# Performance work log

Hardware: AMD Instinct MI355X
Metric: run time of the kernel (lower is better)

Reference implementation:

```python
import jax, jax.numpy as jnp
import numpy as np

N = 30000      # nodes
IN = 768       # input feature dim
C = 128        # hidden channels (= conv out_dim, = gate dim)
HEADS = 4      # attention heads (TransformerConv and Semantic)
DH = 128       # per-head dim (concat=False -> out_channels)
R = 3          # num relations
E = 80000      # edges per relation
NEG = 0.01     # LeakyReLU slope


def setup_inputs() -> dict:
    key = jax.random.key(0)
    ks = iter(jax.random.split(key, 64))
    def nx(shape):
        return jax.random.normal(next(ks), shape, dtype=jnp.float32) * 0.02
    inp = {}
    inp["x"] = jax.random.normal(next(ks), (N, IN), dtype=jnp.float32)
    inp["edges"] = jax.random.randint(next(ks), (R, 2, E), 0, N, dtype=jnp.int32)
    inp["lin1_W"] = nx((IN, C)); inp["lin1_b"] = jnp.zeros((C,), jnp.float32)
    for l in ("l1", "l2"):
        inp[f"{l}_Wq"] = nx((R, C, HEADS * DH)); inp[f"{l}_bq"] = jnp.zeros((R, HEADS * DH), jnp.float32)
        inp[f"{l}_Wk"] = nx((R, C, HEADS * DH)); inp[f"{l}_bk"] = jnp.zeros((R, HEADS * DH), jnp.float32)
        inp[f"{l}_Wv"] = nx((R, C, HEADS * DH)); inp[f"{l}_bv"] = jnp.zeros((R, HEADS * DH), jnp.float32)
        inp[f"{l}_Ws"] = nx((R, C, DH));         inp[f"{l}_bs"] = jnp.zeros((R, DH), jnp.float32)
        inp[f"{l}_gW"] = nx((C + DH, C));        inp[f"{l}_gb"] = jnp.zeros((C,), jnp.float32)
        inp[f"{l}_sW1"] = nx((HEADS, C, C));     inp[f"{l}_sb1"] = jnp.zeros((HEADS, C), jnp.float32)
        inp[f"{l}_sw2"] = nx((HEADS, C))
    inp["lin2_W"] = nx((C, C)); inp["lin2_b"] = jnp.zeros((C,), jnp.float32)
    inp["clf_W"] = nx((C, 2)); inp["clf_b"] = jnp.zeros((2,), jnp.float32)
    return inp


def lrelu(x):
    return jnp.where(x >= 0, x, NEG * x)


def transformer_conv(x, src, dst, Wq, bq, Wk, bk, Wv, bv, Ws, bs):
    # PyG TransformerConv, heads=HEADS, concat=False (head mean), root_weight=True, eval (no dropout)
    n = x.shape[0]
    q = (x @ Wq + bq).reshape(n, HEADS, DH)
    k = (x @ Wk + bk).reshape(n, HEADS, DH)
    v = (x @ Wv + bv).reshape(n, HEADS, DH)
    logits = (q[dst] * k[src]).sum(-1) / np.sqrt(DH)      # [E, H]
    m = jax.ops.segment_max(logits, dst, num_segments=n)  # scatter-softmax (stable)
    a = jnp.exp(logits - m[dst])
    s = jax.ops.segment_sum(a, dst, num_segments=n)
    alpha = a / s[dst]
    agg = jax.ops.segment_sum(alpha[:, :, None] * v[src], dst, num_segments=n)  # [N, H, DH]
    return agg.mean(axis=1) + x @ Ws + bs


def semantic(Hm, sW1, sb1, sw2):
    # Hm: [N, R, C]; per-head scoring MLP -> softmax over relations -> weighted sum, averaged over heads
    t = jnp.tanh(jnp.einsum('nrc,hco->hnro', Hm, sW1) + sb1[:, None, None, :])  # [H, N, R, C]
    scores = jnp.einsum('hnro,ho->hnr', t, sw2).mean(axis=1)                    # [H, R]
    beta = jax.nn.softmax(scores, axis=-1)
    return jnp.einsum('hr,nrc->nc', beta, Hm) / HEADS


def rgt_layer(x, edges, Wq, bq, Wk, bk, Wv, bv, Ws, bs, gW, gb, sW1, sb1, sw2):
    Hs = []
    for r in range(R):  # small fixed relation loop
        src, dst = edges[r, 0], edges[r, 1]
        U = transformer_conv(x, src, dst, Wq[r], bq[r], Wk[r], bk[r], Wv[r], bv[r], Ws[r], bs[r])
        Z = jax.nn.sigmoid(jnp.concatenate([U, x], axis=1) @ gW + gb)
        Hs.append(jnp.tanh(U) * Z + x * (1.0 - Z))
    Hm = jnp.stack(Hs, axis=1)  # [N, R, C]
    return semantic(Hm, sW1, sb1, sw2)


def reference(x, edges, lin1_W, lin1_b,
              l1_Wq, l1_bq, l1_Wk, l1_bk, l1_Wv, l1_bv, l1_Ws, l1_bs, l1_gW, l1_gb, l1_sW1, l1_sb1, l1_sw2,
              l2_Wq, l2_bq, l2_Wk, l2_bk, l2_Wv, l2_bv, l2_Ws, l2_bs, l2_gW, l2_gb, l2_sW1, l2_sb1, l2_sw2,
              lin2_W, lin2_b, clf_W, clf_b):
    h = lrelu(x @ lin1_W + lin1_b)
    h = rgt_layer(h, edges, l1_Wq, l1_bq, l1_Wk, l1_bk, l1_Wv, l1_bv, l1_Ws, l1_bs, l1_gW, l1_gb, l1_sW1, l1_sb1, l1_sw2)
    h = rgt_layer(h, edges, l2_Wq, l2_bq, l2_Wk, l2_bk, l2_Wv, l2_bv, l2_Ws, l2_bs, l2_gW, l2_gb, l2_sW1, l2_sb1, l2_sw2)
    h = lrelu(h @ lin2_W + lin2_b)
    return h @ clf_W + clf_b
```

## Files before the change

kernel.cpp:

```cpp
#include <hip/hip_runtime.h>
#include <math.h>

#define Nn 30000
#define RR 3
#define EE 80000
#define MT_M 235

#define SAP 72
#define SAP2 136
#define EP_LD 70
#define KBIG 0x40000000

typedef __attribute__((ext_vector_type(8))) short bf16x8;
typedef __attribute__((ext_vector_type(4))) float f32x4;

__device__ __forceinline__ unsigned short f2bf(float f) {
    union { float f; unsigned u; } v; v.f = f;
    unsigned r = v.u + 0x7fff + ((v.u >> 16) & 1);
    return (unsigned short)(r >> 16);
}
__device__ __forceinline__ float fast_tanh(float x) {
    float e = __expf(2.f * x);
    return 1.f - 2.f / (e + 1.f);
}
__device__ __forceinline__ void unpack8(uint4 u, float* f) {
    union { unsigned u; float f; } a;
    a.u = u.x << 16;          f[0] = a.f;
    a.u = u.x & 0xffff0000u;  f[1] = a.f;
    a.u = u.y << 16;          f[2] = a.f;
    a.u = u.y & 0xffff0000u;  f[3] = a.f;
    a.u = u.z << 16;          f[4] = a.f;
    a.u = u.z & 0xffff0000u;  f[5] = a.f;
    a.u = u.w << 16;          f[6] = a.f;
    a.u = u.w & 0xffff0000u;  f[7] = a.f;
}

__device__ __forceinline__ void mfma_core(
    const short* __restrict__ A, int lda,
    const short* __restrict__ A2, int lda2, int ksplit,
    const short* __restrict__ Bt,
    int M, int K, int m0, int n0,
    short* As, short* Bs, f32x4 (&acc)[4][4])
{
    const int t = threadIdx.x;
    const int srow = t >> 3;
    const int scol = (t & 7) << 3;
    const int lane = t & 63;
    const int wave = t >> 6;
    const int wm = (wave >> 1) << 6;
    const int wn = (wave & 1) << 6;
    const int fr = lane & 15;
    const int quad = lane >> 4;

    for (int k0 = 0; k0 < K; k0 += 64) {
        const short* Abase; int kk0, ldax;
        if (k0 < ksplit) { Abase = A;  kk0 = k0;          ldax = lda;  }
        else             { Abase = A2; kk0 = k0 - ksplit; ldax = lda2; }
        #pragma unroll
        for (int rr = 0; rr < 4; rr++) {
            int r = srow + rr * 32;
            int gr = m0 + r;
            bf16x8 va = {0, 0, 0, 0, 0, 0, 0, 0};
            if (gr < M) va = *(const bf16x8*)(Abase + (size_t)gr * ldax + kk0 + scol);
            *(bf16x8*)(As + r * SAP + scol) = va;
        }
        #pragma unroll
        for (int rr = 0; rr < 4; rr++) {
            int r = srow + rr * 32;
            bf16x8 vb = *(const bf16x8*)(Bt + (size_t)(n0 + r) * K + k0 + scol);
            *(bf16x8*)(Bs + r * SAP + scol) = vb;
        }
        __syncthreads();
        #pragma unroll
        for (int kc = 0; kc < 2; kc++) {
            bf16x8 af[4], bfr[4];
            #pragma unroll
            for (int i = 0; i < 4; i++)
                af[i] = *(const bf16x8*)(As + (wm + i * 16 + fr) * SAP + kc * 32 + quad * 8);
            #pragma unroll
            for (int i = 0; i < 4; i++)
                bfr[i] = *(const bf16x8*)(Bs + (wn + i * 16 + fr) * SAP + kc * 32 + quad * 8);
            #pragma unroll
            for (int mi = 0; mi < 4; mi++)
                #pragma unroll
                for (int ni = 0; ni < 4; ni++)
                    acc[mi][ni] = __builtin_amdgcn_mfma_f32_16x16x32_bf16(
                        af[mi], bfr[ni], acc[mi][ni], 0, 0, 0);
        }
        __syncthreads();
    }
}

__global__ __launch_bounds__(256) void gemm_mfma(
    const short* __restrict__ A, int lda,
    const short* __restrict__ A2, int lda2, int ksplit,
    const short* __restrict__ Bt, const float* __restrict__ bias,
    float* __restrict__ C, int ldc, short* __restrict__ Cbf, int ldcbf,
    int M, int K, int act)
{
    __shared__ short As[128 * SAP];
    __shared__ short Bs[128 * SAP];
    f32x4 acc[4][4];
    #pragma unroll
    for (int i = 0; i < 4; i++)
        #pragma unroll
        for (int j = 0; j < 4; j++) acc[i][j] = (f32x4){0.f, 0.f, 0.f, 0.f};
    int m0 = blockIdx.y * 128, n0 = blockIdx.x * 128;
    mfma_core(A, lda, A2, lda2, ksplit, Bt, M, K, m0, n0, As, Bs, acc);

    const int t = threadIdx.x;
    const int lane = t & 63, wave = t >> 6;
    const int wm = (wave >> 1) << 6, wn = (wave & 1) << 6;
    const int fr = lane & 15, quad = lane >> 4;
    float* ws = (float*)As + wave * 16 * EP_LD;
    const int rrow = lane >> 2;
    const int cseg = (lane & 3) << 4;
    #pragma unroll
    for (int mi = 0; mi < 4; mi++) {
        #pragma unroll
        for (int ni = 0; ni < 4; ni++)
            #pragma unroll
            for (int reg = 0; reg < 4; reg++)
                ws[(quad * 4 + reg) * EP_LD + ni * 16 + fr] = acc[mi][ni][reg];
        int gr = m0 + wm + mi * 16 + rrow;
        if (gr >= M) continue;
        int gc = n0 + wn + cseg;
        float vals[16];
        #pragma unroll
        for (int j = 0; j < 16; j++) {
            float v = ws[rrow * EP_LD + cseg + j] + bias[gc + j];
            if (act == 1) v = (v >= 0.f) ? v : 0.01f * v;
            vals[j] = v;
        }
        if (C) {
            float* cp = C + (size_t)gr * ldc + gc;
            #pragma unroll
            for (int j4 = 0; j4 < 4; j4++)
                *(float4*)(cp + j4 * 4) = make_float4(vals[j4 * 4], vals[j4 * 4 + 1],
                                                      vals[j4 * 4 + 2], vals[j4 * 4 + 3]);
        }
        if (Cbf) {
            unsigned pk[8];
            #pragma unroll
            for (int j2 = 0; j2 < 8; j2++)
                pk[j2] = ((unsigned)f2bf(vals[2 * j2 + 1]) << 16) | (unsigned)f2bf(vals[2 * j2]);
            unsigned* bp = (unsigned*)(Cbf + (size_t)gr * ldcbf + gc);
            *(uint4*)bp       = make_uint4(pk[0], pk[1], pk[2], pk[3]);
            *(uint4*)(bp + 4) = make_uint4(pk[4], pk[5], pk[6], pk[7]);
        }
    }
}

__global__ __launch_bounds__(256) void gemm_lin1(
    const float* __restrict__ A, int lda,
    const short* __restrict__ Bt, const float* __restrict__ bias,
    float* __restrict__ C, int ldc, short* __restrict__ Cbf, int ldcbf,
    int M, int K, int act)
{
    __shared__ short As[128 * SAP];
    __shared__ short Bs[128 * SAP];
    f32x4 acc[4][4];
    #pragma unroll
    for (int i = 0; i < 4; i++)
        #pragma unroll
        for (int j = 0; j < 4; j++) acc[i][j] = (f32x4){0.f, 0.f, 0.f, 0.f};
    int m0 = blockIdx.y * 128, n0 = blockIdx.x * 128;

    const int t = threadIdx.x;
    const int srow = t >> 3;
    const int scol = (t & 7) << 3;
    const int lane = t & 63;
    const int wave = t >> 6;
    const int wm = (wave >> 1) << 6;
    const int wn = (wave & 1) << 6;
    const int fr = lane & 15;
    const int quad = lane >> 4;

    for (int k0 = 0; k0 < K; k0 += 64) {
        #pragma unroll
        for (int rr = 0; rr < 4; rr++) {
            int r = srow + rr * 32;
            int gr = m0 + r;
            unsigned pk[4] = {0, 0, 0, 0};
            if (gr < M) {
                const float* ap = A + (size_t)gr * lda + k0 + scol;
                float4 f0 = *(const float4*)ap;
                float4 f1 = *(const float4*)(ap + 4);
                pk[0] = ((unsigned)f2bf(f0.y) << 16) | (unsigned)f2bf(f0.x);
                pk[1] = ((unsigned)f2bf(f0.w) << 16) | (unsigned)f2bf(f0.z);
                pk[2] = ((unsigned)f2bf(f1.y) << 16) | (unsigned)f2bf(f1.x);
                pk[3] = ((unsigned)f2bf(f1.w) << 16) | (unsigned)f2bf(f1.z);
            }
            *(uint4*)(As + r * SAP + scol) = make_uint4(pk[0], pk[1], pk[2], pk[3]);
        }
        #pragma unroll
        for (int rr = 0; rr < 4; rr++) {
            int r = srow + rr * 32;
            bf16x8 vb = *(const bf16x8*)(Bt + (size_t)(n0 + r) * K + k0 + scol);
            *(bf16x8*)(Bs + r * SAP + scol) = vb;
        }
        __syncthreads();
        #pragma unroll
        for (int kc = 0; kc < 2; kc++) {
            bf16x8 af[4], bfr[4];
            #pragma unroll
            for (int i = 0; i < 4; i++)
                af[i] = *(const bf16x8*)(As + (wm + i * 16 + fr) * SAP + kc * 32 + quad * 8);
            #pragma unroll
            for (int i = 0; i < 4; i++)
                bfr[i] = *(const bf16x8*)(Bs + (wn + i * 16 + fr) * SAP + kc * 32 + quad * 8);
            #pragma unroll
            for (int mi = 0; mi < 4; mi++)
                #pragma unroll
                for (int ni = 0; ni < 4; ni++)
                    acc[mi][ni] = __builtin_amdgcn_mfma_f32_16x16x32_bf16(
                        af[mi], bfr[ni], acc[mi][ni], 0, 0, 0);
        }
        __syncthreads();
    }

    float* ws = (float*)As + wave * 16 * EP_LD;
    const int rrow = lane >> 2;
    const int cseg = (lane & 3) << 4;
    #pragma unroll
    for (int mi = 0; mi < 4; mi++) {
        #pragma unroll
        for (int ni = 0; ni < 4; ni++)
            #pragma unroll
            for (int reg = 0; reg < 4; reg++)
                ws[(quad * 4 + reg) * EP_LD + ni * 16 + fr] = acc[mi][ni][reg];
        int gr = m0 + wm + mi * 16 + rrow;
        if (gr >= M) continue;
        int gc = n0 + wn + cseg;
        float vals[16];
        #pragma unroll
        for (int j = 0; j < 16; j++) {
            float v = ws[rrow * EP_LD + cseg + j] + bias[gc + j];
            if (act == 1) v = (v >= 0.f) ? v : 0.01f * v;
            vals[j] = v;
        }
        float* cp = C + (size_t)gr * ldc + gc;
        #pragma unroll
        for (int j4 = 0; j4 < 4; j4++)
            *(float4*)(cp + j4 * 4) = make_float4(vals[j4 * 4], vals[j4 * 4 + 1],
                                                  vals[j4 * 4 + 2], vals[j4 * 4 + 3]);
        unsigned pk[8];
        #pragma unroll
        for (int j2 = 0; j2 < 8; j2++)
            pk[j2] = ((unsigned)f2bf(vals[2 * j2 + 1]) << 16) | (unsigned)f2bf(vals[2 * j2]);
        unsigned* bp = (unsigned*)(Cbf + (size_t)gr * ldcbf + gc);
        *(uint4*)bp       = make_uint4(pk[0], pk[1], pk[2], pk[3]);
        *(uint4*)(bp + 4) = make_uint4(pk[4], pk[5], pk[6], pk[7]);
    }
}

__global__ __launch_bounds__(256) void gemm_qkvs(
    const short* __restrict__ A,
    const short* __restrict__ Wt, const float* __restrict__ bias,
    short* __restrict__ qkv3, short* __restrict__ Ubf, int M)
{
    __shared__ short As[128 * SAP];
    __shared__ short Bs[128 * SAP];
    f32x4 acc[4][4];
    #pragma unroll
    for (int i = 0; i < 4; i++)
        #pragma unroll
        for (int j = 0; j < 4; j++) acc[i][j] = (f32x4){0.f, 0.f, 0.f, 0.f};
    int m0 = blockIdx.y * 128, bx = blockIdx.x, n0 = bx * 128;
    mfma_core(A, 128, A, 128, KBIG, Wt, M, 128, m0, n0, As, Bs, acc);

    const int t = threadIdx.x;
    const int lane = t & 63, wave = t >> 6;
    const int wm = (wave >> 1) << 6, wn = (wave & 1) << 6;
    const int fr = lane & 15, quad = lane >> 4;
    float* ws = (float*)As + wave * 16 * EP_LD;
    const int rrow = lane >> 2;
    const int cseg = (lane & 3) << 4;
    #pragma unroll
    for (int mi = 0; mi < 4; mi++) {
        #pragma unroll
        for (int ni = 0; ni < 4; ni++)
            #pragma unroll
            for (int reg = 0; reg < 4; reg++)
                ws[(quad * 4 + reg) * EP_LD + ni * 16 + fr] = acc[mi][ni][reg];
        int gr = m0 + wm + mi * 16 + rrow;
        if (gr >= M) continue;
        int lc = wn + cseg;
        float vals[16];
        #pragma unroll
        for (int j = 0; j < 16; j++)
            vals[j] = ws[rrow * EP_LD + cseg + j] + bias[n0 + lc + j];
        unsigned pk[8];
        #pragma unroll
        for (int j2 = 0; j2 < 8; j2++)
            pk[j2] = ((unsigned)f2bf(vals[2 * j2 + 1]) << 16) | (unsigned)f2bf(vals[2 * j2]);
        short* dst;
        if (bx < 36) {
            int r = bx / 12;
            dst = qkv3 + ((size_t)(r * Nn + gr)) * 1536 + (bx - r * 12) * 128 + lc;
        } else {
            dst = Ubf + (size_t)gr * 384 + (bx - 36) * 128 + lc;
        }
        unsigned* bp = (unsigned*)dst;
        *(uint4*)bp       = make_uint4(pk[0], pk[1], pk[2], pk[3]);
        *(uint4*)(bp + 4) = make_uint4(pk[4], pk[5], pk[6], pk[7]);
    }
}

__global__ __launch_bounds__(256) void gate_sem(
    const short* __restrict__ Ubf,
    const short* __restrict__ Hbf,
    const short* __restrict__ gWt, const float* __restrict__ gb,
    const float* __restrict__ Hf,
    const short* __restrict__ sW1t,
    const float* __restrict__ sb1, const float* __restrict__ sw2,
    float* __restrict__ Hm,
    float* __restrict__ partial, int M)
{
    __shared__ short L0[128 * 144];
    __shared__ short HmT[128 * SAP2];
    __shared__ float redL[16];
    short* As = L0;
    short* Bs = L0 + 128 * SAP;

    f32x4 acc[4][4];
    #pragma unroll
    for (int i = 0; i < 4; i++)
        #pragma unroll
        for (int j = 0; j < 4; j++) acc[i][j] = (f32x4){0.f, 0.f, 0.f, 0.f};
    int r = blockIdx.z;
    int m0 = blockIdx.y * 128;
    mfma_core(Ubf + r * 128, 384, Hbf, 128, 128, gWt, M, 256, m0, 0, As, Bs, acc);

    const int t = threadIdx.x;
    const int srow = t >> 3;
    const int scol = (t & 7) << 3;
    const int lane = t & 63, wave = t >> 6;
    const int wm = (wave >> 1) << 6, wn = (wave & 1) << 6;
    const int fr = lane & 15, quad = lane >> 4;
    float* ws = (float*)As + wave * 16 * EP_LD;
    const int rrow = lane >> 2;
    const int cseg = (lane & 3) << 4;

    #pragma unroll
    for (int mi = 0; mi < 4; mi++) {
        #pragma unroll
        for (int ni = 0; ni < 4; ni++)
            #pragma unroll
            for (int reg = 0; reg < 4; reg++)
                ws[(quad * 4 + reg) * EP_LD + ni * 16 + fr] = acc[mi][ni][reg];
        int row = wm + mi * 16 + rrow;
        int gr = m0 + row;
        int gc = wn + cseg;
        unsigned pk[8] = {0, 0, 0, 0, 0, 0, 0, 0};
        if (gr < M) {
            const short* up = Ubf + (size_t)gr * 384 + r * 128 + gc;
            const float* hp = Hf + (size_t)gr * 128 + gc;
            float uv[16], hv[16];
            uint4 u0 = *(const uint4*)up;
            uint4 u1 = *(const uint4*)(up + 8);
            unpack8(u0, uv); unpack8(u1, uv + 8);
            #pragma unroll
            for (int j4 = 0; j4 < 4; j4++)
                *(float4*)(hv + j4 * 4) = *(const float4*)(hp + j4 * 4);
            float vals[16];
            #pragma unroll
            for (int j = 0; j < 16; j++) {
                float g = ws[rrow * EP_LD + cseg + j] + gb[gc + j];
                float z = 1.f / (1.f + __expf(-g));
                vals[j] = fast_tanh(uv[j]) * z + hv[j] * (1.f - z);
            }
            float* cp = Hm + (size_t)gr * 384 + r * 128 + gc;
            #pragma unroll
            for (int j4 = 0; j4 < 4; j4++)
                *(float4*)(cp + j4 * 4) = make_float4(vals[j4 * 4], vals[j4 * 4 + 1],
                                                      vals[j4 * 4 + 2], vals[j4 * 4 + 3]);
            #pragma unroll
            for (int j2 = 0; j2 < 8; j2++)
                pk[j2] = ((unsigned)f2bf(vals[2 * j2 + 1]) << 16) | (unsigned)f2bf(vals[2 * j2]);
        }
        unsigned* hp2 = (unsigned*)(HmT + row * SAP2 + gc);
        *(uint4*)hp2       = make_uint4(pk[0], pk[1], pk[2], pk[3]);
        *(uint4*)(hp2 + 4) = make_uint4(pk[4], pk[5], pk[6], pk[7]);
    }

    for (int h = 0; h < 4; h++) {
        __syncthreads();
        const short* Bh = sW1t + (size_t)h * 128 * 128;
        #pragma unroll
        for (int rr2 = 0; rr2 < 4; rr2++) {
            int n = srow + rr2 * 32;
            #pragma unroll
            for (int half = 0; half < 2; half++) {
                bf16x8 vb = *(const bf16x8*)(Bh + n * 128 + half * 64 + scol);
                *(bf16x8*)(L0 + n * SAP2 + half * 64 + scol) = vb;
            }
        }
        __syncthreads();
        f32x4 acc2[4][4];
        #pragma unroll
        for (int i = 0; i < 4; i++)
            #pragma unroll
            for (int j = 0; j < 4; j++) acc2[i][j] = (f32x4){0.f, 0.f, 0.f, 0.f};
        #pragma unroll
        for (int kc = 0; kc < 4; kc++) {
            bf16x8 af[4], bfr[4];
            #pragma unroll
            for (int i = 0; i < 4; i++)
                af[i] = *(const bf16x8*)(HmT + (wm + i * 16 + fr) * SAP2 + kc * 32 + quad * 8);
            #pragma unroll
            for (int i = 0; i < 4; i++)
                bfr[i] = *(const bf16x8*)(L0 + (wn + i * 16 + fr) * SAP2 + kc * 32 + quad * 8);
            #pragma unroll
            for (int mi = 0; mi < 4; mi++)
                #pragma unroll
                for (int ni = 0; ni < 4; ni++)
                    acc2[mi][ni] = __builtin_amdgcn_mfma_f32_16x16x32_bf16(
                        af[mi], bfr[ni], acc2[mi][ni], 0, 0, 0);
        }
        float local = 0.f;
        #pragma unroll
        for (int ni = 0; ni < 4; ni++) {
            int gcl = h * 128 + wn + ni * 16 + fr;
            float b = sb1[gcl], w2 = sw2[gcl];
            #pragma unroll
            for (int mi = 0; mi < 4; mi++) {
                #pragma unroll
                for (int reg = 0; reg < 4; reg++) {
                    int gr = m0 + wm + mi * 16 + quad * 4 + reg;
                    if (gr < M) local += fast_tanh(acc2[mi][ni][reg] + b) * w2;
                }
            }
        }
        #pragma unroll
        for (int off = 1; off < 64; off <<= 1) local += __shfl_xor(local, off);
        if (lane == 0) redL[h * 4 + wave] = local;
    }
    __syncthreads();
    if (t < 4) {
        float s = redL[t * 4] + redL[t * 4 + 1] + redL[t * 4 + 2] + redL[t * 4 + 3];
        partial[(t * 3 + r) * MT_M + blockIdx.y] = s;
    }
}

__global__ void compute_w2(const float* __restrict__ partial, float* __restrict__ w, float invN)
{
    int t = threadIdx.x;
    float sz[12];
    #pragma unroll
    for (int z = 0; z < 12; z++) {
        float s = 0.f;
        for (int i = t; i < MT_M; i += 64) s += partial[z * MT_M + i];
        #pragma unroll
        for (int off = 1; off < 64; off <<= 1) s += __shfl_xor(s, off);
        sz[z] = s;
    }
    if (t == 0) {
        float wr[3] = {0.f, 0.f, 0.f};
        for (int h = 0; h < 4; h++) {
            float s0 = sz[h * 3 + 0] * invN;
            float s1 = sz[h * 3 + 1] * invN;
            float s2 = sz[h * 3 + 2] * invN;
            float mx = fmaxf(s0, fmaxf(s1, s2));
            float e0 = __expf(s0 - mx), e1 = __expf(s1 - mx), e2 = __expf(s2 - mx);
            float inv = 1.f / (e0 + e1 + e2);
            wr[0] += 0.25f * e0 * inv;
            wr[1] += 0.25f * e1 * inv;
            wr[2] += 0.25f * e2 * inv;
        }
        w[0] = wr[0]; w[1] = wr[1]; w[2] = wr[2];
    }
}

__global__ void mix_kernel(const float* __restrict__ Hm, const float* __restrict__ w,
                           float* __restrict__ h, short* __restrict__ hbf, int total4)
{
    int i = blockIdx.x * blockDim.x + threadIdx.x;
    if (i >= total4) return;
    int n = i >> 5, c4 = (i & 31) << 2;
    const float* row = Hm + (size_t)n * 384 + c4;
    float4 a = *(const float4*)row;
    float4 b = *(const float4*)(row + 128);
    float4 c = *(const float4*)(row + 256);
    float w0 = w[0], w1 = w[1], w2 = w[2];
    float4 v = make_float4(w0 * a.x + w1 * b.x + w2 * c.x,
                           w0 * a.y + w1 * b.y + w2 * c.y,
                           w0 * a.z + w1 * b.z + w2 * c.z,
                           w0 * a.w + w1 * b.w + w2 * c.w);
    *(float4*)(h + (size_t)n * 128 + c4) = v;
    unsigned p0 = ((unsigned)f2bf(v.y) << 16) | (unsigned)f2bf(v.x);
    unsigned p1 = ((unsigned)f2bf(v.w) << 16) | (unsigned)f2bf(v.z);
    *(uint2*)(hbf + (size_t)n * 128 + c4) = make_uint2(p0, p1);
}

__global__ void prep_global_kernel(const float* __restrict__ lin1_W, const float* __restrict__ lin2_W,
                                   short* __restrict__ lin1Wt, short* __restrict__ lin2Wt)
{
    int id = blockIdx.x * blockDim.x + threadIdx.x;
    if (id < 98304) {
        int n = id / 768, k = id % 768;
        lin1Wt[id] = (short)f2bf(lin1_W[k * 128 + n]);
    } else if (id < 114688) {
        int r = id - 98304;
        int n = r / 128, k = r % 128;
        lin2Wt[r] = (short)f2bf(lin2_W[k * 128 + n]);
    }
}

__global__ void prep_layer_kernel(
    const float* __restrict__ Wq, const float* __restrict__ Wk, const float* __restrict__ Wv,
    const float* __restrict__ Ws, const float* __restrict__ bq, const float* __restrict__ bk,
    const float* __restrict__ bv, const float* __restrict__ bs,
    const float* __restrict__ gW, const float* __restrict__ sW1,
    short* __restrict__ qkvsWt, short* __restrict__ gWt,
    short* __restrict__ sW1t, float* __restrict__ qkvsB)
{
    const int S0 = 638976;
    const int S1 = S0 + 32768;
    const int S2 = S1 + 65536;
    const int S3 = S2 + 4992;
    int id = blockIdx.x * blockDim.x + threadIdx.x;
    if (id < S0) {
        int n = id / 128, k = id - n * 128;
        float v;
        if (n < 4608) {
            int r = n / 1536, j = n - r * 1536;
            if (j < 512)       v = Wq[(size_t)r * 65536 + k * 512 + j];
            else if (j < 1024) v = Wk[(size_t)r * 65536 + k * 512 + (j - 512)];
            else               v = Wv[(size_t)r * 65536 + k * 512 + (j - 1024)];
        } else {
            int m = n - 4608;
            int r = m / 128, c = m - r * 128;
            v = Ws[(size_t)r * 16384 + k * 128 + c];
        }
        qkvsWt[id] = (short)f2bf(v);
    } else if (id < S1) {
        int q = id - S0;
        int n = q / 256, k = q - n * 256;
        gWt[q] = (short)f2bf(gW[k * 128 + n]);
    } else if (id < S2) {
        int q = id - S1;
        int h = q / 16384, rem = q - h * 16384;
        int n = rem / 128, k = rem - n * 128;
        sW1t[q] = (short)f2bf(sW1[(size_t)h * 16384 + k * 128 + n]);
    } else if (id < S3) {
        int q = id - S2;
        float v;
        if (q < 4608) {
            int r = q / 1536, j = q - r * 1536;
            if (j < 512)       v = bq[r * 512 + j];
            else if (j < 1024) v = bk[r * 512 + (j - 512)];
            else               v = bv[r * 512 + (j - 1024)];
        } else {
            v = bs[q - 4608];
        }
        qkvsB[q] = v;
    }
}

__global__ void zero_i32_kernel(int* __restrict__ p, int n)
{
    int i = blockIdx.x * blockDim.x + threadIdx.x;
    if (i < n) p[i] = 0;
}

__global__ void hist3_kernel(const int* __restrict__ edges, int* __restrict__ cnt3)
{
    int i = blockIdx.x * blockDim.x + threadIdx.x;
    if (i >= 3 * EE) return;
    int r = i / EE, e = i - r * EE;
    int d = edges[(size_t)r * 2 * EE + EE + e];
    atomicAdd(&cnt3[r * Nn + d], 1);
}

__global__ __launch_bounds__(1024) void scan3_kernel(const int* __restrict__ cnt3,
                                                     int* __restrict__ rowptr3)
{
    __shared__ int part[1024];
    const int r = blockIdx.x;
    const int* cnt = cnt3 + r * Nn;
    int* rowptr = rowptr3 + r * (Nn + 1);
    int tid = threadIdx.x;
    int per = (Nn + 1023) >> 10;
    int base = tid * per;
    int s = 0;
    for (int i = 0; i < per; i++) {
        int idx = base + i;
        if (idx < Nn) s += cnt[idx];
    }
    part[tid] = s;
    __syncthreads();
    for (int off = 1; off < 1024; off <<= 1) {
        int val = (tid >= off) ? part[tid - off] : 0;
        __syncthreads();
        part[tid] += val;
        __syncthreads();
    }
    int excl = (tid == 0) ? 0 : part[tid - 1];
    for (int i = 0; i < per; i++) {
        int idx = base + i;
        if (idx < Nn) { rowptr[idx] = excl; excl += cnt[idx]; }
    }
    if (tid == 1023) rowptr[Nn] = part[1023];
}

__global__ void scatter3_kernel(const int* __restrict__ edges,
                                const int* __restrict__ rowptr3, int* __restrict__ fill3,
                                int* __restrict__ col3)
{
    int i = blockIdx.x * blockDim.x + threadIdx.x;
    if (i >= 3 * EE) return;
    int r = i / EE, e = i - r * EE;
    int src = edges[(size_t)r * 2 * EE + e];
    int d   = edges[(size_t)r * 2 * EE + EE + e];
    int pos = rowptr3[r * (Nn + 1) + d] + atomicAdd(&fill3[r * Nn + d], 1);
    col3[r * EE + pos] = src;
}

__global__ __launch_bounds__(256) void attn_kernel(
    const short* __restrict__ qkv3,
    const int* __restrict__ rowptr3, const int* __restrict__ col3,
    short* __restrict__ Ubf)
{
    int wid = ((blockIdx.x * blockDim.x + threadIdx.x) >> 6);
    int lane = threadIdx.x & 63;
    if (wid >= 3 * Nn) return;
    int r = wid / Nn, n = wid - r * Nn;
    const short* qkv = qkv3 + (size_t)r * Nn * 1536;
    const int* rowptr = rowptr3 + r * (Nn + 1);
    const int* colb = col3 + r * EE;
    int beg = rowptr[n], end = rowptr[n + 1];

    uint4 qv = ((const uint4*)(qkv + (size_t)n * 1536))[lane];
    float qf[8];
    unpack8(qv, qf);

    float m = -INFINITY, s = 0.f;
    float acc[8] = {0.f, 0.f, 0.f, 0.f, 0.f, 0.f, 0.f, 0.f};
    const float scale = 0.088388347648318447f;

    for (int i = beg; i < end; i++) {
        int src = colb[i];
        const short* base = qkv + (size_t)src * 1536;
        uint4 kv4 = ((const uint4*)(base + 512))[lane];
        uint4 vv4 = ((const uint4*)(base + 1024))[lane];
        float kf[8];
        unpack8(kv4, kf);
        float p = qf[0] * kf[0] + qf[1] * kf[1] + qf[2] * kf[2] + qf[3] * kf[3]
                + qf[4] * kf[4] + qf[5] * kf[5] + qf[6] * kf[6] + qf[7] * kf[7];
        p += __shfl_xor(p, 1);
        p += __shfl_xor(p, 2);
        p += __shfl_xor(p, 4);
        p += __shfl_xor(p, 8);
        float l = p * scale;
        float nm = fmaxf(m, l);
        float sc = __expf(m - nm);
        float pe = __expf(l - nm);
        float vf[8];
        unpack8(vv4, vf);
        s = s * sc + pe;
        #pragma unroll
        for (int j = 0; j < 8; j++) acc[j] = acc[j] * sc + pe * vf[j];
        m = nm;
    }

    float inv = (s > 0.f) ? 1.f / s : 0.f;
    #pragma unroll
    for (int j = 0; j < 8; j++) acc[j] *= inv;
    #pragma unroll
    for (int j = 0; j < 8; j++) acc[j] += __shfl_xor(acc[j], 16);
    #pragma unroll
    for (int j = 0; j < 8; j++) acc[j] += __shfl_xor(acc[j], 32);

    if (lane < 16) {
        short* urow = Ubf + (size_t)n * 384 + r * 128 + lane * 8;
        uint4 old = *(uint4*)urow;
        float sv[8];
        unpack8(old, sv);
        #pragma unroll
        for (int j = 0; j < 8; j++) sv[j] += 0.25f * acc[j];
        unsigned p0 = ((unsigned)f2bf(sv[1]) << 16) | (unsigned)f2bf(sv[0]);
        unsigned p1 = ((unsigned)f2bf(sv[3]) << 16) | (unsigned)f2bf(sv[2]);
        unsigned p2 = ((unsigned)f2bf(sv[5]) << 16) | (unsigned)f2bf(sv[4]);
        unsigned p3 = ((unsigned)f2bf(sv[7]) << 16) | (unsigned)f2bf(sv[6]);
        *(uint4*)urow = make_uint4(p0, p1, p2, p3);
    }
}

__global__ void clf_kernel(const float* __restrict__ t, const float* __restrict__ W,
                           const float* __restrict__ b, float* __restrict__ out, int M)
{
    int n = blockIdx.x * blockDim.x + threadIdx.x;
    if (n >= M) return;
    const float* row = t + (size_t)n * 128;
    float a0 = b[0], a1 = b[1];
    #pragma unroll
    for (int kk = 0; kk < 128; kk++) {
        float a = row[kk];
        a0 += a * W[kk * 2];
        a1 += a * W[kk * 2 + 1];
    }
    out[n * 2] = a0;
    out[n * 2 + 1] = a1;
}

extern "C" void kernel_launch(void* const* d_in, const int* in_sizes, int n_in,
                              void* d_out, int out_size, void* d_ws, size_t ws_size,
                              hipStream_t stream)
{
    const float* x      = (const float*)d_in[0];
    const int*   edges  = (const int*)d_in[1];
    const float* lin1_W = (const float*)d_in[2];
    const float* lin1_b = (const float*)d_in[3];
    const int L0 = 4, L1 = 17;
    const float* lin2_W = (const float*)d_in[30];
    const float* lin2_b = (const float*)d_in[31];
    const float* clf_W  = (const float*)d_in[32];
    const float* clf_b  = (const float*)d_in[33];
    float* out = (float*)d_out;

    char* w = (char*)d_ws;
    size_t off = 0;
    auto alloc = [&](size_t bytes) { void* p = w + off; off = (off + bytes + 255) & ~(size_t)255; return p; };
    float* h      = (float*)alloc((size_t)Nn * 128 * 4);
    short* h_bf   = (short*)alloc((size_t)Nn * 128 * 2);
    short* U_bf   = (short*)alloc((size_t)Nn * 384 * 2);
    char* BIG     = (char*)alloc((size_t)3 * Nn * 1536 * 2);
    short* qkv3   = (short*)BIG;
    float* Hm     = (float*)BIG;
    float* lin2o  = (float*)BIG;
    short* lin1Wt = (short*)alloc((size_t)98304 * 2);
    short* lin2Wt = (short*)alloc((size_t)16384 * 2);
    short* qkvsWt = (short*)alloc((size_t)2 * 638976 * 2);
    short* gWt    = (short*)alloc((size_t)2 * 32768 * 2);
    short* sW1t   = (short*)alloc((size_t)2 * 65536 * 2);
    float* qkvsB  = (float*)alloc((size_t)2 * 4992 * 4);
    int* rowptr3  = (int*)alloc((size_t)3 * (Nn + 1) * 4);
    int* cnt3     = (int*)alloc((size_t)3 * Nn * 4);
    int* col3     = (int*)alloc((size_t)3 * EE * 4);
    float* partial = (float*)alloc((size_t)12 * MT_M * 4);
    float* wmix   = (float*)alloc(3 * 4);

    const int MT = MT_M;
    dim3 blk(256);

    {
        prep_global_kernel<<<(114688 + 255) / 256, blk, 0, stream>>>(lin1_W, lin2_W, lin1Wt, lin2Wt);
        for (int l = 0; l < 2; l++) {
            int base = (l == 0) ? L0 : L1;
            prep_layer_kernel<<<(742272 + 255) / 256, blk, 0, stream>>>(
                (const float*)d_in[base + 0], (const float*)d_in[base + 2], (const float*)d_in[base + 4],
                (const float*)d_in[base + 6], (const float*)d_in[base + 1], (const float*)d_in[base + 3],
                (const float*)d_in[base + 5], (const float*)d_in[base + 7],
                (const float*)d_in[base + 8], (const float*)d_in[base + 10],
                qkvsWt + (size_t)l * 638976, gWt + (size_t)l * 32768,
                sW1t + (size_t)l * 65536, qkvsB + (size_t)l * 4992);
        }
        zero_i32_kernel<<<(3 * Nn + 255) / 256, blk, 0, stream>>>(cnt3, 3 * Nn);
        hist3_kernel<<<(3 * EE + 255) / 256, blk, 0, stream>>>(edges, cnt3);
        scan3_kernel<<<3, 1024, 0, stream>>>(cnt3, rowptr3);
        zero_i32_kernel<<<(3 * Nn + 255) / 256, blk, 0, stream>>>(cnt3, 3 * Nn);
        scatter3_kernel<<<(3 * EE + 255) / 256, blk, 0, stream>>>(edges, rowptr3, cnt3, col3);
    }

    gemm_lin1<<<dim3(1, MT), blk, 0, stream>>>(
        x, 768, lin1Wt, lin1_b, h, 128, h_bf, 128, Nn, 768, 1);

    for (int l = 0; l < 2; l++) {
        int base = (l == 0) ? L0 : L1;
        const float* gb  = (const float*)d_in[base + 9];
        const float* sb1 = (const float*)d_in[base + 11];
        const float* sw2 = (const float*)d_in[base + 12];
        short* lqkvsWt = qkvsWt + (size_t)l * 638976;
        short* lgWt    = gWt + (size_t)l * 32768;
        short* lsW1t   = sW1t + (size_t)l * 65536;
        float* lqkvsB  = qkvsB + (size_t)l * 4992;

        gemm_qkvs<<<dim3(39, MT), blk, 0, stream>>>(
            h_bf, lqkvsWt, lqkvsB, qkv3, U_bf, Nn);

        attn_kernel<<<(3 * Nn + 3) / 4, blk, 0, stream>>>(qkv3, rowptr3, col3, U_bf);

        gate_sem<<<dim3(1, MT, 3), blk, 0, stream>>>(
            U_bf, h_bf, lgWt, gb, h, lsW1t, sb1, sw2, Hm, partial, Nn);

        compute_w2<<<1, 64, 0, stream>>>(partial, wmix, 1.f / (float)Nn);
        mix_kernel<<<(Nn * 32 + 255) / 256, blk, 0, stream>>>(Hm, wmix, h, h_bf, Nn * 32);
    }

    gemm_mfma<<<dim3(1, MT), blk, 0, stream>>>(
        h_bf, 128, h_bf, 128, KBIG, lin2Wt, lin2_b, lin2o, 128, (short*)nullptr, 0, Nn, 128, 1);
    clf_kernel<<<(Nn + 255) / 256, blk, 0, stream>>>(lin2o, clf_W, clf_b, out, Nn);
}
```

Measured before the change: 984.9 us.

## Read GEMM weights directly from global memory and store Hm in bf16

In gemm_qkvs and gate_sem, only the activation tile is staged through shared memory. The weight fragments are now loaded straight from global memory (expected to hit cache), which removes the B staging, its shared-memory footprint and the extra syncs in the sW1 head loop. The intermediate Hm tensor is now written in bf16 instead of fp32, so gate_sem writes and mix_kernel reads half the bytes, with a small loss of precision. Lower shared-memory use may raise occupancy, but uncoalesced direct global weight reads could cost latency.

```diff
diff --git a/kernel.cpp b/kernel.cpp
--- a/kernel.cpp
+++ b/kernel.cpp
@@ -260,19 +260,50 @@
     short* __restrict__ qkv3, short* __restrict__ Ubf, int M)
 {
     __shared__ short As[128 * SAP];
-    __shared__ short Bs[128 * SAP];
     f32x4 acc[4][4];
     #pragma unroll
     for (int i = 0; i < 4; i++)
         #pragma unroll
         for (int j = 0; j < 4; j++) acc[i][j] = (f32x4){0.f, 0.f, 0.f, 0.f};
     int m0 = blockIdx.y * 128, bx = blockIdx.x, n0 = bx * 128;
-    mfma_core(A, 128, A, 128, KBIG, Wt, M, 128, m0, n0, As, Bs, acc);
 
     const int t = threadIdx.x;
+    const int srow = t >> 3;
+    const int scol = (t & 7) << 3;
     const int lane = t & 63, wave = t >> 6;
     const int wm = (wave >> 1) << 6, wn = (wave & 1) << 6;
     const int fr = lane & 15, quad = lane >> 4;
+
+    for (int k0 = 0; k0 < 128; k0 += 64) {
+        #pragma unroll
+        for (int rr = 0; rr < 4; rr++) {
+            int r = srow + rr * 32;
+            int gr = m0 + r;
+            bf16x8 va = {0, 0, 0, 0, 0, 0, 0, 0};
+            if (gr < M) va = *(const bf16x8*)(A + (size_t)gr * 128 + k0 + scol);
+            *(bf16x8*)(As + r * SAP + scol) = va;
+        }
+        __syncthreads();
+        #pragma unroll
+        for (int kc = 0; kc < 2; kc++) {
+            bf16x8 af[4], bfr[4];
+            #pragma unroll
+            for (int i = 0; i < 4; i++)
+                af[i] = *(const bf16x8*)(As + (wm + i * 16 + fr) * SAP + kc * 32 + quad * 8);
+            #pragma unroll
+            for (int i = 0; i < 4; i++)
+                bfr[i] = *(const bf16x8*)(Wt + (size_t)(n0 + wn + i * 16 + fr) * 128
+                                          + k0 + kc * 32 + quad * 8);
+            #pragma unroll
+            for (int mi = 0; mi < 4; mi++)
+                #pragma unroll
+                for (int ni = 0; ni < 4; ni++)
+                    acc[mi][ni] = __builtin_amdgcn_mfma_f32_16x16x32_bf16(
+                        af[mi], bfr[ni], acc[mi][ni], 0, 0, 0);
+        }
+        __syncthreads();
+    }
+
     float* ws = (float*)As + wave * 16 * EP_LD;
     const int rrow = lane >> 2;
     const int cseg = (lane & 3) << 4;
@@ -314,14 +345,12 @@
     const float* __restrict__ Hf,
     const short* __restrict__ sW1t,
     const float* __restrict__ sb1, const float* __restrict__ sw2,
-    float* __restrict__ Hm,
+    short* __restrict__ HmBf,
     float* __restrict__ partial, int M)
 {
-    __shared__ short L0[128 * 144];
+    __shared__ short As[128 * SAP];
     __shared__ short HmT[128 * SAP2];
     __shared__ float redL[16];
-    short* As = L0;
-    short* Bs = L0 + 128 * SAP;
 
     f32x4 acc[4][4];
     #pragma unroll
@@ -330,7 +359,6 @@
         for (int j = 0; j < 4; j++) acc[i][j] = (f32x4){0.f, 0.f, 0.f, 0.f};
     int r = blockIdx.z;
     int m0 = blockIdx.y * 128;
-    mfma_core(Ubf + r * 128, 384, Hbf, 128, 128, gWt, M, 256, m0, 0, As, Bs, acc);
 
     const int t = threadIdx.x;
     const int srow = t >> 3;
@@ -338,6 +366,40 @@
     const int lane = t & 63, wave = t >> 6;
     const int wm = (wave >> 1) << 6, wn = (wave & 1) << 6;
     const int fr = lane & 15, quad = lane >> 4;
+
+    for (int k0 = 0; k0 < 256; k0 += 64) {
+        const short* Abase; int kk0, ldax;
+        if (k0 < 128) { Abase = Ubf + r * 128; kk0 = k0;       ldax = 384; }
+        else          { Abase = Hbf;           kk0 = k0 - 128; ldax = 128; }
+        #pragma unroll
+        for (int rr = 0; rr < 4; rr++) {
+            int rw = srow + rr * 32;
+            int gr = m0 + rw;
+            bf16x8 va = {0, 0, 0, 0, 0, 0, 0, 0};
+            if (gr < M) va = *(const bf16x8*)(Abase + (size_t)gr * ldax + kk0 + scol);
+            *(bf16x8*)(As + rw * SAP + scol) = va;
+        }
+        __syncthreads();
+        #pragma unroll
+        for (int kc = 0; kc < 2; kc++) {
+            bf16x8 af[4], bfr[4];
+            #pragma unroll
+            for (int i = 0; i < 4; i++)
+                af[i] = *(const bf16x8*)(As + (wm + i * 16 + fr) * SAP + kc * 32 + quad * 8);
+            #pragma unroll
+            for (int i = 0; i < 4; i++)
+                bfr[i] = *(const bf16x8*)(gWt + (size_t)(wn + i * 16 + fr) * 256
+                                          + k0 + kc * 32 + quad * 8);
+            #pragma unroll
+            for (int mi = 0; mi < 4; mi++)
+                #pragma unroll
+                for (int ni = 0; ni < 4; ni++)
+                    acc[mi][ni] = __builtin_amdgcn_mfma_f32_16x16x32_bf16(
+                        af[mi], bfr[ni], acc[mi][ni], 0, 0, 0);
+        }
+        __syncthreads();
+    }
+
     float* ws = (float*)As + wave * 16 * EP_LD;
     const int rrow = lane >> 2;
     const int cseg = (lane & 3) << 4;
@@ -370,33 +432,22 @@
                 float z = 1.f / (1.f + __expf(-g));
                 vals[j] = fast_tanh(uv[j]) * z + hv[j] * (1.f - z);
             }
-            float* cp = Hm + (size_t)gr * 384 + r * 128 + gc;
-            #pragma unroll
-            for (int j4 = 0; j4 < 4; j4++)
-                *(float4*)(cp + j4 * 4) = make_float4(vals[j4 * 4], vals[j4 * 4 + 1],
-                                                      vals[j4 * 4 + 2], vals[j4 * 4 + 3]);
             #pragma unroll
             for (int j2 = 0; j2 < 8; j2++)
                 pk[j2] = ((unsigned)f2bf(vals[2 * j2 + 1]) << 16) | (unsigned)f2bf(vals[2 * j2]);
+            unsigned* bp = (unsigned*)(HmBf + (size_t)gr * 384 + r * 128 + gc);
+            *(uint4*)bp       = make_uint4(pk[0], pk[1], pk[2], pk[3]);
+            *(uint4*)(bp + 4) = make_uint4(pk[4], pk[5], pk[6], pk[7]);
         }
         unsigned* hp2 = (unsigned*)(HmT + row * SAP2 + gc);
         *(uint4*)hp2       = make_uint4(pk[0], pk[1], pk[2], pk[3]);
         *(uint4*)(hp2 + 4) = make_uint4(pk[4], pk[5], pk[6], pk[7]);
     }
-
+    __syncthreads();
+
+    #pragma unroll
     for (int h = 0; h < 4; h++) {
-        __syncthreads();
         const short* Bh = sW1t + (size_t)h * 128 * 128;
-        #pragma unroll
-        for (int rr2 = 0; rr2 < 4; rr2++) {
-            int n = srow + rr2 * 32;
-            #pragma unroll
-            for (int half = 0; half < 2; half++) {
-                bf16x8 vb = *(const bf16x8*)(Bh + n * 128 + half * 64 + scol);
-                *(bf16x8*)(L0 + n * SAP2 + half * 64 + scol) = vb;
-            }
-        }
-        __syncthreads();
         f32x4 acc2[4][4];
         #pragma unroll
         for (int i = 0; i < 4; i++)
@@ -410,7 +461,8 @@
                 af[i] = *(const bf16x8*)(HmT + (wm + i * 16 + fr) * SAP2 + kc * 32 + quad * 8);
             #pragma unroll
             for (int i = 0; i < 4; i++)
-                bfr[i] = *(const bf16x8*)(L0 + (wn + i * 16 + fr) * SAP2 + kc * 32 + quad * 8);
+                bfr[i] = *(const bf16x8*)(Bh + (size_t)(wn + i * 16 + fr) * 128
+                                          + kc * 32 + quad * 8);
             #pragma unroll
             for (int mi = 0; mi < 4; mi++)
                 #pragma unroll
@@ -472,25 +524,29 @@
     }
 }
 
-__global__ void mix_kernel(const float* __restrict__ Hm, const float* __restrict__ w,
-                           float* __restrict__ h, short* __restrict__ hbf, int total4)
+__global__ void mix_kernel(const short* __restrict__ HmBf, const float* __restrict__ w,
+                           float* __restrict__ h, short* __restrict__ hbf, int total8)
 {
     int i = blockIdx.x * blockDim.x + threadIdx.x;
-    if (i >= total4) return;
-    int n = i >> 5, c4 = (i & 31) << 2;
-    const float* row = Hm + (size_t)n * 384 + c4;
-    float4 a = *(const float4*)row;
-    float4 b = *(const float4*)(row + 128);
-    float4 c = *(const float4*)(row + 256);
+    if (i >= total8) return;
+    int n = i >> 4, c8 = (i & 15) << 3;
+    const short* row = HmBf + (size_t)n * 384 + c8;
+    float a[8], b[8], c[8];
+    unpack8(*(const uint4*)row, a);
+    unpack8(*(const uint4*)(row + 128), b);
+    unpack8(*(const uint4*)(row + 256), c);
     float w0 = w[0], w1 = w[1], w2 = w[2];
-    float4 v = make_float4(w0 * a.x + w1 * b.x + w2 * c.x,
-                           w0 * a.y + w1 * b.y + w2 * c.y,
-                           w0 * a.z + w1 * b.z + w2 * c.z,
-                           w0 * a.w + w1 * b.w + w2 * c.w);
-    *(float4*)(h + (size_t)n * 128 + c4) = v;
-    unsigned p0 = ((unsigned)f2bf(v.y) << 16) | (unsigned)f2bf(v.x);
-    unsigned p1 = ((unsigned)f2bf(v.w) << 16) | (unsigned)f2bf(v.z);
-    *(uint2*)(hbf + (size_t)n * 128 + c4) = make_uint2(p0, p1);
+    float v[8];
+    #pragma unroll
+    for (int j = 0; j < 8; j++) v[j] = w0 * a[j] + w1 * b[j] + w2 * c[j];
+    float* hp = h + (size_t)n * 128 + c8;
+    *(float4*)hp       = make_float4(v[0], v[1], v[2], v[3]);
+    *(float4*)(hp + 4) = make_float4(v[4], v[5], v[6], v[7]);
+    unsigned p0 = ((unsigned)f2bf(v[1]) << 16) | (unsigned)f2bf(v[0]);
+    unsigned p1 = ((unsigned)f2bf(v[3]) << 16) | (unsigned)f2bf(v[2]);
+    unsigned p2 = ((unsigned)f2bf(v[5]) << 16) | (unsigned)f2bf(v[4]);
+    unsigned p3 = ((unsigned)f2bf(v[7]) << 16) | (unsigned)f2bf(v[6]);
+    *(uint4*)(hbf + (size_t)n * 128 + c8) = make_uint4(p0, p1, p2, p3);
 }
 
 __global__ void prep_global_kernel(const float* __restrict__ lin1_W, const float* __restrict__ lin2_W,
@@ -727,7 +783,7 @@
     short* U_bf   = (short*)alloc((size_t)Nn * 384 * 2);
     char* BIG     = (char*)alloc((size_t)3 * Nn * 1536 * 2);
     short* qkv3   = (short*)BIG;
-    float* Hm     = (float*)BIG;
+    short* HmBf   = (short*)BIG;
     float* lin2o  = (float*)BIG;
     short* lin1Wt = (short*)alloc((size_t)98304 * 2);
     short* lin2Wt = (short*)alloc((size_t)16384 * 2);
@@ -782,10 +838,10 @@
         attn_kernel<<<(3 * Nn + 3) / 4, blk, 0, stream>>>(qkv3, rowptr3, col3, U_bf);
 
         gate_sem<<<dim3(1, MT, 3), blk, 0, stream>>>(
-            U_bf, h_bf, lgWt, gb, h, lsW1t, sb1, sw2, Hm, partial, Nn);
+            U_bf, h_bf, lgWt, gb, h, lsW1t, sb1, sw2, HmBf, partial, Nn);
 
         compute_w2<<<1, 64, 0, stream>>>(partial, wmix, 1.f / (float)Nn);
-        mix_kernel<<<(Nn * 32 + 255) / 256, blk, 0, stream>>>(Hm, wmix, h, h_bf, Nn * 32);
+        mix_kernel<<<(Nn * 16 + 255) / 256, blk, 0, stream>>>(HmBf, wmix, h, h_bf, Nn * 16);
     }
 
     gemm_mfma<<<dim3(1, MT), blk, 0, stream>>>(
```

New measurement: 1.077 ms. +9.3%, slower.
